# Optimization experiments

Measured on AMD Instinct MI355X. Metric: run time of the kernel, lower is better.

The kernel has to match this reference:

```python
import jax, jax.numpy as jnp
import numpy as np

LN_EPS = 1e-5

def _conv2d(x, w, b, pad):
    # x: [B,C,H,W], w: [O,I,kh,kw] -> [B,O,H,W]
    y = jax.lax.conv_general_dilated(
        x, w, window_strides=(1, 1), padding=[(pad, pad), (pad, pad)],
        dimension_numbers=('NCHW', 'OIHW', 'NCHW'))
    return y + b[None, :, None, None]

def setup_inputs() -> dict:
    key = jax.random.key(0)
    ks = jax.random.split(key, 12)
    B, C, H, W = 4, 256, 64, 64
    D = 64  # inner_projection
    s_in = 1.0 / np.sqrt(C)
    s_d1 = 1.0 / np.sqrt(D)
    s_d3 = 1.0 / np.sqrt(D * 9)
    return {
        'x':     jax.random.normal(ks[0], (B, C, H, W), jnp.float32),
        'w_in':  jax.random.normal(ks[1], (D, C, 1, 1), jnp.float32) * s_in,
        'b_in':  jnp.zeros((D,), jnp.float32),
        'wq':    jax.random.normal(ks[2], (D, D, 3, 3), jnp.float32) * s_d3,
        'bq':    jnp.zeros((D,), jnp.float32),
        'wk':    jax.random.normal(ks[3], (D, D, 3, 3), jnp.float32) * s_d3,
        'bk':    jnp.zeros((D,), jnp.float32),
        'wv':    jax.random.normal(ks[4], (D, D, 3, 3), jnp.float32) * s_d3,
        'bv':    jnp.zeros((D,), jnp.float32),
        'w_out': jax.random.normal(ks[5], (C, D, 1, 1), jnp.float32) * s_d1,
        'b_out': jnp.zeros((C,), jnp.float32),
        'gamma': jax.random.normal(ks[6], (1,), jnp.float32) * 0.1,
        'ln_w':  jnp.ones((C,), jnp.float32),
        'ln_b':  jnp.zeros((C,), jnp.float32),
    }

def _attention(q, k, v):
    # full-pixel attention, NO 1/sqrt(d) scale (matches source)
    B, C, H, W = v.shape
    N = H * W
    qf = q.reshape(B, -1, N)   # [B,d,N]
    kf = k.reshape(B, -1, N)
    vf = v.reshape(B, -1, N)
    energy = jnp.einsum('bci,bcj->bij', qf, kf)      # [B,N,N] = Q^T K
    attn = jax.nn.softmax(energy, axis=-1)
    out = jnp.einsum('bcj,bij->bci', vf, attn)        # V @ attn^T
    return out.reshape(B, C, H, W)

def _layernorm2d(x, w, b):
    # normalize over channel dim per pixel (LayerNorm2d)
    mu = jnp.mean(x, axis=1, keepdims=True)
    var = jnp.var(x, axis=1, keepdims=True)
    xn = (x - mu) * jax.lax.rsqrt(var + LN_EPS)
    return xn * w[None, :, None, None] + b[None, :, None, None]

def reference(x, w_in, b_in, wq, bq, wk, bk, wv, bv, w_out, b_out, gamma, ln_w, ln_b):
    att = _conv2d(x, w_in, b_in, 0)          # inner projection [B,D,H,W]
    q = _conv2d(att, wq, bq, 1)
    k = _conv2d(att, wk, bk, 1)
    v = _conv2d(att, wv, bv, 1)
    att = _attention(q, k, v)
    att = _conv2d(att, w_out, b_out, 0)       # outer projection [B,C,H,W]
    return _layernorm2d(gamma * x + att, ln_w, ln_b)
```

## Files before the change

### kernel.cpp

```cpp
#include <hip/hip_runtime.h>
#include <hip/hip_bf16.h>

#define BB 4
#define CC 256
#define DD 64
#define HH 64
#define WW 64
#define NN 4096
#define NSPLIT 4
#define SM_SHIFT2 92.332482616893664f
#define LOG2E 1.4426950408889634f

typedef __hip_bfloat16 bf16;
typedef __attribute__((ext_vector_type(8))) short bf16x8;
typedef __attribute__((ext_vector_type(4))) float f32x4;
typedef __attribute__((ext_vector_type(4))) short s16x4;

#define MFMA16(a, b, c) __builtin_amdgcn_mfma_f32_16x16x32_bf16(a, b, c, 0, 0, 0)

#if __has_builtin(__builtin_amdgcn_mfma_f32_16x16x16bf16_1k)
static __device__ __forceinline__ f32x4 MFMA16K(s16x4 a, s16x4 b, f32x4 c) {
  return __builtin_amdgcn_mfma_f32_16x16x16bf16_1k(a, b, c, 0, 0, 0);
}
#else
static __device__ __forceinline__ f32x4 MFMA16K(s16x4 a, s16x4 b, f32x4 c) {
  f32x4 d;
  asm("v_mfma_f32_16x16x16_bf16 %0, %1, %2, %3"
      : "=&v"(d) : "v"(a), "v"(b), "v"(c));
  return d;
}
#endif

#if __has_builtin(__builtin_amdgcn_exp2f)
#define EXP2F(x) __builtin_amdgcn_exp2f(x)
#else
#define EXP2F(x) exp2f(x)
#endif

static __device__ __forceinline__ float ldin(const void* p, size_t i, bool isb) {
  return isb ? __bfloat162float(((const bf16*)p)[i]) : ((const float*)p)[i];
}
static __device__ __forceinline__ void stout(void* p, size_t i, float v, bool isb) {
  if (isb) ((bf16*)p)[i] = __float2bfloat16(v);
  else     ((float*)p)[i] = v;
}
static __device__ __forceinline__ unsigned pack2(bf16 a, bf16 b) {
  unsigned short ua = *reinterpret_cast<unsigned short*>(&a);
  unsigned short ub = *reinterpret_cast<unsigned short*>(&b);
  return (unsigned)ua | ((unsigned)ub << 16);
}
static __device__ __forceinline__ bool probe_bf16(const unsigned* lnw) {
  return lnw[0] == 0x3F803F80u;
}

__global__ __launch_bounds__(256) void k_wt(
    const void* __restrict__ wq, const void* __restrict__ wk,
    const void* __restrict__ wv, const void* __restrict__ w_in,
    const void* __restrict__ w_out,
    bf16* __restrict__ Wth, bf16* __restrict__ Wtl,
    bf16* __restrict__ Win_h, bf16* __restrict__ Win_l,
    bf16* __restrict__ Wo_h, bf16* __restrict__ Wo_l,
    const unsigned* __restrict__ lnw) {
  const bool isb = probe_bf16(lnw);
  int u = blockIdx.x * 256 + threadIdx.x;
  if (u < 110592) {
    int c3 = u / 36864, rem = u % 36864;
    int tap = rem / 4096, r2 = rem % 4096;
    int oc = r2 >> 6, ic = r2 & 63;
    const void* w = (c3 == 0) ? wq : ((c3 == 1) ? wk : wv);
    float v = ldin(w, (size_t)oc * 576 + ic * 9 + tap, isb);
    bf16 h = __float2bfloat16(v);
    Wth[u] = h;
    Wtl[u] = __float2bfloat16(v - __bfloat162float(h));
  } else if (u < 126976) {
    int v2 = u - 110592;
    float v = ldin(w_in, v2, isb);
    bf16 h = __float2bfloat16(v);
    Win_h[v2] = h;
    Win_l[v2] = __float2bfloat16(v - __bfloat162float(h));
  } else {
    int v2 = u - 126976;
    float v = ldin(w_out, v2, isb);
    bf16 h = __float2bfloat16(v);
    Wo_h[v2] = h;
    Wo_l[v2] = __float2bfloat16(v - __bfloat162float(h));
  }
}

__global__ __launch_bounds__(256) void k_conv_in(
    const void* __restrict__ x,
    const bf16* __restrict__ Win_h, const bf16* __restrict__ Win_l,
    const void* __restrict__ bias, bf16* __restrict__ att_h,
    bf16* __restrict__ att_l, const unsigned* __restrict__ lnw) {
  __shared__ __align__(16) short Xh[32 * 64];
  __shared__ __align__(16) short Xl[32 * 64];
  const bool isb = probe_bf16(lnw);
  const int b = blockIdx.y, n0 = blockIdx.x * 32;
  const int t = threadIdx.x;
  const int w = t >> 6, lane = t & 63, quad = lane >> 4, l16 = lane & 15;
  const int l7 = l16 & 7;
  const size_t xoff = (size_t)b * CC * NN;
  f32x4 acc[2];
  #pragma unroll
  for (int nt = 0; nt < 2; ++nt)
    #pragma unroll
    for (int r = 0; r < 4; ++r)
      acc[nt][r] = ldin(bias, w * 16 + quad * 4 + r, isb);
  for (int c0 = 0; c0 < CC; c0 += 64) {
    __syncthreads();
    #pragma unroll
    for (int i = 0; i < 4; ++i) {
      int u = t + i * 256;
      int dd = u >> 5, n = u & 31;
      float v0 = ldin(x, xoff + (size_t)(c0 + 2 * dd) * NN + n0 + n, isb);
      float v1 = ldin(x, xoff + (size_t)(c0 + 2 * dd + 1) * NN + n0 + n, isb);
      bf16 h0 = __float2bfloat16(v0), h1 = __float2bfloat16(v1);
      bf16 l0 = __float2bfloat16(v0 - __bfloat162float(h0));
      bf16 l1 = __float2bfloat16(v1 - __bfloat162float(h1));
      int cs = ((dd >> 2) ^ (n & 7)) * 8 + ((2 * dd) & 7);
      *(unsigned*)&Xh[n * 64 + cs] = pack2(h0, h1);
      *(unsigned*)&Xl[n * 64 + cs] = pack2(l0, l1);
    }
    __syncthreads();
    #pragma unroll
    for (int kc = 0; kc < 2; ++kc) {
      size_t woff = (size_t)(w * 16 + l16) * 256 + c0 + kc * 32 + quad * 8;
      bf16x8 wh = *(const bf16x8*)(Win_h + woff);
      bf16x8 wl = *(const bf16x8*)(Win_l + woff);
      const int xo = ((kc * 4 + quad) ^ l7) * 8;
      #pragma unroll
      for (int nt = 0; nt < 2; ++nt) {
        int rn = nt * 16 + l16;
        bf16x8 xh = *(const bf16x8*)&Xh[rn * 64 + xo];
        bf16x8 xl = *(const bf16x8*)&Xl[rn * 64 + xo];
        acc[nt] = MFMA16(wh, xh, acc[nt]);
        acc[nt] = MFMA16(wh, xl, acc[nt]);
        acc[nt] = MFMA16(wl, xh, acc[nt]);
      }
    }
  }
  #pragma unroll
  for (int nt = 0; nt < 2; ++nt) {
    size_t off = ((size_t)b * NN + n0 + nt * 16 + l16) * DD + w * 16 + quad * 4;
    bf16 h[4], l[4];
    #pragma unroll
    for (int r = 0; r < 4; ++r) {
      float v = acc[nt][r];
      h[r] = __float2bfloat16(v);
      l[r] = __float2bfloat16(v - __bfloat162float(h[r]));
    }
    *(uint2*)&att_h[off] = make_uint2(pack2(h[0], h[1]), pack2(h[2], h[3]));
    *(uint2*)&att_l[off] = make_uint2(pack2(l[0], l[1]), pack2(l[2], l[3]));
  }
}

__global__ __launch_bounds__(256) void k_conv3(
    const bf16* __restrict__ att_h, const bf16* __restrict__ att_l,
    const bf16* __restrict__ Wth, const bf16* __restrict__ Wtl,
    const void* __restrict__ bq, const void* __restrict__ bk,
    const void* __restrict__ bv,
    bf16* __restrict__ qth, bf16* __restrict__ qtl,
    bf16* __restrict__ kth, bf16* __restrict__ ktl,
    bf16* __restrict__ vt, const unsigned* __restrict__ lnw) {
  __shared__ __align__(16) short Ah[3 * 66 * 64];
  __shared__ __align__(16) short Al[3 * 66 * 64];
  float* o_s = reinterpret_cast<float*>(Ah);
  const bool isb = probe_bf16(lnw);
  const int y = blockIdx.x, b = blockIdx.y;
  const int t = threadIdx.x;
  const int w = t >> 6, lane = t & 63, quad = lane >> 4, l16 = lane & 15;
  const uint4 z4 = make_uint4(0, 0, 0, 0);
  #pragma unroll
  for (int r = 0; r < 3; ++r) {
    int yp = y + r - 1;
    bool ok = (unsigned)yp < 64u;
    const uint4* sh = (const uint4*)(att_h + ((size_t)b * NN + (size_t)yp * 64) * DD);
    const uint4* sl = (const uint4*)(att_l + ((size_t)b * NN + (size_t)yp * 64) * DD);
    #pragma unroll
    for (int ii = 0; ii < 2; ++ii) {
      int u = t + ii * 256;
      int xx = u >> 3, ch = u & 7;
      int rr = r * 66 + xx + 1;
      uint4 vh = ok ? sh[u] : z4;
      uint4 vl = ok ? sl[u] : z4;
      int cs = (ch ^ (rr & 7)) * 8;
      *(uint4*)&Ah[rr * 64 + cs] = vh;
      *(uint4*)&Al[rr * 64 + cs] = vl;
    }
    if (t < 16) {
      int rr = r * 66 + ((t & 1) ? 65 : 0);
      int cs = (t >> 1) * 8;
      *(uint4*)&Ah[rr * 64 + cs] = z4;
      *(uint4*)&Al[rr * 64 + cs] = z4;
    }
  }
  __syncthreads();
  #pragma unroll 1
  for (int c3 = 0; c3 < 3; ++c3) {
    const void* bp = (c3 == 0) ? bq : ((c3 == 1) ? bk : bv);
    const bf16* wth = Wth + (size_t)c3 * 9 * 4096;
    const bf16* wtl = Wtl + (size_t)c3 * 9 * 4096;
    f32x4 acc[4];
    #pragma unroll
    for (int nt = 0; nt < 4; ++nt)
      #pragma unroll
      for (int r = 0; r < 4; ++r)
        acc[nt][r] = ldin(bp, w * 16 + quad * 4 + r, isb);
    #pragma unroll
    for (int tap = 0; tap < 9; ++tap) {
      const int dy = tap / 3, dx = tap % 3;
      const int woff = tap * 4096 + (w * 16 + l16) * 64 + quad * 8;
      bf16x8 wh0 = *(const bf16x8*)(wth + woff);
      bf16x8 wh1 = *(const bf16x8*)(wth + woff + 32);
      bf16x8 wl0 = *(const bf16x8*)(wtl + woff);
      bf16x8 wl1 = *(const bf16x8*)(wtl + woff + 32);
      #pragma unroll
      for (int nt = 0; nt < 4; ++nt) {
        int rr = dy * 66 + nt * 16 + l16 + dx;
        int chA = (quad ^ (rr & 7)) * 8;
        int chB = ((quad + 4) ^ (rr & 7)) * 8;
        bf16x8 ah0 = *(const bf16x8*)&Ah[rr * 64 + chA];
        bf16x8 ah1 = *(const bf16x8*)&Ah[rr * 64 + chB];
        bf16x8 al0 = *(const bf16x8*)&Al[rr * 64 + chA];
        bf16x8 al1 = *(const bf16x8*)&Al[rr * 64 + chB];
        acc[nt] = MFMA16(wh0, ah0, acc[nt]);
        acc[nt] = MFMA16(wh1, ah1, acc[nt]);
        acc[nt] = MFMA16(wh0, al0, acc[nt]);
        acc[nt] = MFMA16(wh1, al1, acc[nt]);
        acc[nt] = MFMA16(wl0, ah0, acc[nt]);
        acc[nt] = MFMA16(wl1, ah1, acc[nt]);
      }
    }
    if (c3 < 2) {
      bf16* dh = (c3 == 0) ? qth : kth;
      bf16* dl = (c3 == 0) ? qtl : ktl;
      const float qsc = (c3 == 0) ? LOG2E : 1.0f;
      const size_t rowb = (size_t)b * NN + (size_t)y * 64;
      #pragma unroll
      for (int nt = 0; nt < 4; ++nt) {
        size_t off = (rowb + nt * 16 + l16) * DD + w * 16 + quad * 4;
        bf16 h[4], l[4];
        #pragma unroll
        for (int r = 0; r < 4; ++r) {
          float v = acc[nt][r] * qsc;
          h[r] = __float2bfloat16(v);
          l[r] = __float2bfloat16(v - __bfloat162float(h[r]));
        }
        *(uint2*)&dh[off] = make_uint2(pack2(h[0], h[1]), pack2(h[2], h[3]));
        *(uint2*)&dl[off] = make_uint2(pack2(l[0], l[1]), pack2(l[2], l[3]));
      }
    } else {
      __syncthreads();
      #pragma unroll
      for (int nt = 0; nt < 4; ++nt)
        #pragma unroll
        for (int r = 0; r < 4; ++r)
          o_s[(nt * 16 + l16) * 65 + w * 16 + quad * 4 + r] = acc[nt][r];
      __syncthreads();
      #pragma unroll
      for (int i = 0; i < 8; ++i) {
        int u = t + i * 256;
        int c = u >> 5, np = (u & 31) * 2;
        float v0 = o_s[np * 65 + c], v1 = o_s[(np + 1) * 65 + c];
        *(unsigned*)&vt[((size_t)b * DD + c) * NN + (size_t)y * 64 + np] =
            pack2(__float2bfloat16(v0), __float2bfloat16(v1));
      }
    }
  }
}

__global__ __launch_bounds__(256) void k_attn(
    const bf16* __restrict__ qth, const bf16* __restrict__ qtl,
    const bf16* __restrict__ kth, const bf16* __restrict__ ktl,
    const bf16* __restrict__ vt, float* __restrict__ po,
    float* __restrict__ pl) {
  __shared__ __align__(16) short Kh[2][64 * 64];
  __shared__ __align__(16) short Kl[2][64 * 64];
  __shared__ __align__(16) short Vs[2][64 * 64];
  const int b = blockIdx.y, i0 = blockIdx.x * 128, sp = blockIdx.z;
  const int jt0 = sp * (64 / NSPLIT), jt1 = jt0 + (64 / NSPLIT);
  const int t = threadIdx.x;
  const int w = t >> 6, lane = t & 63, quad = lane >> 4, l16 = lane & 15;
  const int l7 = l16 & 7;
  const int xA = (quad ^ l7) * 8;
  const int xB = ((quad + 4) ^ l7) * 8;
  const int sr = t >> 2, m4 = t & 3, sg = m4 * 16;
  const int sc0 = ((2 * m4) ^ (sr & 7)) * 8;
  const int sc1 = ((2 * m4 + 1) ^ (sr & 7)) * 8;
  bf16x8 qf_h0[2], qf_h1[2], qf_l0[2], qf_l1[2];
  #pragma unroll
  for (int is = 0; is < 2; ++is) {
    size_t qoff = ((size_t)b * NN + i0 + is * 64 + w * 16 + l16) * DD + quad * 8;
    qf_h0[is] = *(const bf16x8*)(qth + qoff);
    qf_h1[is] = *(const bf16x8*)(qth + qoff + 32);
    qf_l0[is] = *(const bf16x8*)(qtl + qoff);
    qf_l1[is] = *(const bf16x8*)(qtl + qoff + 32);
  }
  uint4 kh0, kh1, kl0, kl1, vx0, vx1;
  {
    size_t koff = ((size_t)b * NN + jt0 * 64 + sr) * DD + sg;
    kh0 = ((const uint4*)(kth + koff))[0]; kh1 = ((const uint4*)(kth + koff))[1];
    kl0 = ((const uint4*)(ktl + koff))[0]; kl1 = ((const uint4*)(ktl + koff))[1];
    size_t voff = ((size_t)b * DD + sr) * NN + jt0 * 64 + sg;
    vx0 = ((const uint4*)(vt + voff))[0];  vx1 = ((const uint4*)(vt + voff))[1];
  }
  *(uint4*)&Kh[0][sr * 64 + sc0] = kh0;  *(uint4*)&Kh[0][sr * 64 + sc1] = kh1;
  *(uint4*)&Kl[0][sr * 64 + sc0] = kl0;  *(uint4*)&Kl[0][sr * 64 + sc1] = kl1;
  *(uint4*)&Vs[0][sr * 64 + sc0] = vx0;  *(uint4*)&Vs[0][sr * 64 + sc1] = vx1;
  __syncthreads();
  float l_run[2] = {0.f, 0.f};
  f32x4 oacc[4][2] = {};
  int p = 0;
  for (int jt = jt0; jt < jt1; ++jt) {
    if (jt < jt1 - 1) {
      int j0n = (jt + 1) * 64;
      size_t koff = ((size_t)b * NN + j0n + sr) * DD + sg;
      kh0 = ((const uint4*)(kth + koff))[0]; kh1 = ((const uint4*)(kth + koff))[1];
      kl0 = ((const uint4*)(ktl + koff))[0]; kl1 = ((const uint4*)(ktl + koff))[1];
      size_t voff = ((size_t)b * DD + sr) * NN + j0n + sg;
      vx0 = ((const uint4*)(vt + voff))[0];  vx1 = ((const uint4*)(vt + voff))[1];
    }
    const short* khp = Kh[p];
    const short* klp = Kl[p];
    const short* vsp = Vs[p];
    s16x4 pf[2][4];
    float psum[2] = {0.f, 0.f};
    #pragma unroll
    for (int mt = 0; mt < 4; ++mt) {
      int r0 = (mt * 16 + l16) * 64;
      bf16x8 kf_h0 = *(const bf16x8*)&khp[r0 + xA];
      bf16x8 kf_h1 = *(const bf16x8*)&khp[r0 + xB];
      bf16x8 kf_l0 = *(const bf16x8*)&klp[r0 + xA];
      bf16x8 kf_l1 = *(const bf16x8*)&klp[r0 + xB];
      __builtin_amdgcn_s_setprio(1);
      #pragma unroll
      for (int is = 0; is < 2; ++is) {
        f32x4 c = {0.f, 0.f, 0.f, 0.f};
        c = MFMA16(kf_h0, qf_h0[is], c);
        c = MFMA16(kf_h1, qf_h1[is], c);
        c = MFMA16(kf_h0, qf_l0[is], c);
        c = MFMA16(kf_h1, qf_l1[is], c);
        c = MFMA16(kf_l0, qf_h0[is], c);
        c = MFMA16(kf_l1, qf_h1[is], c);
        s16x4 pk;
        float ps = 0.f;
        #pragma unroll
        for (int r = 0; r < 4; ++r) {
          float pexp = EXP2F(c[r] - SM_SHIFT2);
          bf16 ph = __float2bfloat16(pexp);
          ps += __bfloat162float(ph);
          pk[r] = *reinterpret_cast<short*>(&ph);
        }
        psum[is] += ps;
        pf[is][mt] = pk;
      }
      __builtin_amdgcn_s_setprio(0);
    }
    #pragma unroll
    for (int is = 0; is < 2; ++is) {
      float ps = psum[is];
      ps += __shfl_xor(ps, 16, 64);
      ps += __shfl_xor(ps, 32, 64);
      l_run[is] += ps;
    }
    __builtin_amdgcn_s_setprio(1);
    #pragma unroll
    for (int mt = 0; mt < 4; ++mt) {
      int rv = (mt * 16 + l16) * 64;
      #pragma unroll
      for (int kt = 0; kt < 4; ++kt) {
        s16x4 vf = *(const s16x4*)
            &vsp[rv + ((kt * 2 + (quad >> 1)) ^ l7) * 8 + (quad & 1) * 4];
        oacc[mt][0] = MFMA16K(vf, pf[0][kt], oacc[mt][0]);
        oacc[mt][1] = MFMA16K(vf, pf[1][kt], oacc[mt][1]);
      }
    }
    __builtin_amdgcn_s_setprio(0);
    if (jt < jt1 - 1) {
      short* khn = Kh[p ^ 1];
      short* kln = Kl[p ^ 1];
      short* vsn = Vs[p ^ 1];
      *(uint4*)&khn[sr * 64 + sc0] = kh0;  *(uint4*)&khn[sr * 64 + sc1] = kh1;
      *(uint4*)&kln[sr * 64 + sc0] = kl0;  *(uint4*)&kln[sr * 64 + sc1] = kl1;
      *(uint4*)&vsn[sr * 64 + sc0] = vx0;  *(uint4*)&vsn[sr * 64 + sc1] = vx1;
    }
    __syncthreads();
    p ^= 1;
  }
  const size_t SEGC = (size_t)BB * DD * NN;
  #pragma unroll
  for (int is = 0; is < 2; ++is) {
    const int ig = i0 + is * 64 + w * 16 + l16;
    #pragma unroll
    for (int mt = 0; mt < 4; ++mt)
      #pragma unroll
      for (int r = 0; r < 4; ++r) {
        int c = mt * 16 + quad * 4 + r;
        po[(size_t)sp * SEGC + ((size_t)b * DD + c) * NN + ig] = oacc[mt][is][r];
      }
    if (quad == 0) pl[((size_t)sp * BB + b) * NN + ig] = l_run[is];
  }
}

__global__ __launch_bounds__(256) void k_out_ln(
    const float* __restrict__ po, const float* __restrict__ pl,
    const void* __restrict__ x,
    const bf16* __restrict__ Wo_h, const bf16* __restrict__ Wo_l,
    const void* __restrict__ bias, const void* __restrict__ gamma,
    const void* __restrict__ lw, const void* __restrict__ lb,
    void* __restrict__ out, const unsigned* __restrict__ lnw) {
  __shared__ __align__(16) short Ahs[32 * 64];
  __shared__ __align__(16) short Als[32 * 64];
  __shared__ float inv_s[32];
  __shared__ float red1[32 * 4], red2[32 * 4];
  __shared__ float mu_s[32], rs_s[32];
  __shared__ float lw_s[256], lb_s[256];
  const bool isb = probe_bf16(lnw);
  const int b = blockIdx.y, n0 = blockIdx.x * 32;
  const int t = threadIdx.x;
  const int w = t >> 6, lane = t & 63, quad = lane >> 4, l16 = lane & 15;
  const int l7 = l16 & 7;
  const size_t SEGC = (size_t)BB * DD * NN;
  if (t < 32) {
    int i = n0 + t;
    float lsum = 0.f;
    #pragma unroll
    for (int s = 0; s < NSPLIT; ++s) lsum += pl[((size_t)s * BB + b) * NN + i];
    inv_s[t] = 1.f / lsum;
  }
  lw_s[t] = ldin(lw, t, isb);
  lb_s[t] = ldin(lb, t, isb);
  const float g = ldin(gamma, 0, isb);
  __syncthreads();
  #pragma unroll
  for (int i = 0; i < 4; ++i) {
    int u = t + i * 256;
    int dd = u >> 5, n = u & 31;
    size_t base = ((size_t)b * DD + 2 * dd) * NN + n0 + n;
    float v0 = 0.f, v1 = 0.f;
    #pragma unroll
    for (int s = 0; s < NSPLIT; ++s) {
      v0 += po[(size_t)s * SEGC + base];
      v1 += po[(size_t)s * SEGC + base + NN];
    }
    float inv = inv_s[n];
    v0 *= inv; v1 *= inv;
    bf16 h0 = __float2bfloat16(v0), h1 = __float2bfloat16(v1);
    bf16 l0 = __float2bfloat16(v0 - __bfloat162float(h0));
    bf16 l1 = __float2bfloat16(v1 - __bfloat162float(h1));
    int cs = ((dd >> 2) ^ (n & 7)) * 8 + ((2 * dd) & 7);
    *(unsigned*)&Ahs[n * 64 + cs] = pack2(h0, h1);
    *(unsigned*)&Als[n * 64 + cs] = pack2(l0, l1);
  }
  f32x4 acc[4][2];
  #pragma unroll
  for (int oct = 0; oct < 4; ++oct)
    #pragma unroll
    for (int r = 0; r < 4; ++r) {
      float bo = ldin(bias, w * 64 + oct * 16 + quad * 4 + r, isb);
      #pragma unroll
      for (int nt = 0; nt < 2; ++nt) acc[oct][nt][r] = bo;
    }
  __syncthreads();
  #pragma unroll
  for (int oct = 0; oct < 4; ++oct) {
    const int base = w * 64 + oct * 16;
    #pragma unroll
    for (int kc = 0; kc < 2; ++kc) {
      size_t woff = (size_t)(base + l16) * 64 + kc * 32 + quad * 8;
      bf16x8 wh = *(const bf16x8*)(Wo_h + woff);
      bf16x8 wl = *(const bf16x8*)(Wo_l + woff);
      const int xo = ((kc * 4 + quad) ^ l7) * 8;
      #pragma unroll
      for (int nt = 0; nt < 2; ++nt) {
        int rn = nt * 16 + l16;
        bf16x8 ah = *(const bf16x8*)&Ahs[rn * 64 + xo];
        bf16x8 al = *(const bf16x8*)&Als[rn * 64 + xo];
        acc[oct][nt] = MFMA16(wh, ah, acc[oct][nt]);
        acc[oct][nt] = MFMA16(wh, al, acc[oct][nt]);
        acc[oct][nt] = MFMA16(wl, ah, acc[oct][nt]);
      }
    }
  }
  #pragma unroll
  for (int nt = 0; nt < 2; ++nt) {
    int nn = nt * 16 + l16;
    float s1 = 0.f, s2 = 0.f;
    #pragma unroll
    for (int oct = 0; oct < 4; ++oct)
      #pragma unroll
      for (int r = 0; r < 4; ++r) {
        int oc = w * 64 + oct * 16 + quad * 4 + r;
        float xv = ldin(x, ((size_t)b * CC + oc) * NN + n0 + nn, isb);
        float y = acc[oct][nt][r] + g * xv;
        acc[oct][nt][r] = y;
        s1 += y; s2 += y * y;
      }
    s1 += __shfl_xor(s1, 16, 64); s1 += __shfl_xor(s1, 32, 64);
    s2 += __shfl_xor(s2, 16, 64); s2 += __shfl_xor(s2, 32, 64);
    if (quad == 0) { red1[nn * 4 + w] = s1; red2[nn * 4 + w] = s2; }
  }
  __syncthreads();
  if (t < 32) {
    float sm = red1[t * 4] + red1[t * 4 + 1] + red1[t * 4 + 2] + red1[t * 4 + 3];
    float sq = red2[t * 4] + red2[t * 4 + 1] + red2[t * 4 + 2] + red2[t * 4 + 3];
    float mu = sm * (1.f / 256.f);
    float var = sq * (1.f / 256.f) - mu * mu;
    mu_s[t] = mu;
    rs_s[t] = rsqrtf(var + 1e-5f);
  }
  __syncthreads();
  #pragma unroll
  for (int nt = 0; nt < 2; ++nt) {
    int nn = nt * 16 + l16;
    float mu = mu_s[nn], rs = rs_s[nn];
    #pragma unroll
    for (int oct = 0; oct < 4; ++oct)
      #pragma unroll
      for (int r = 0; r < 4; ++r) {
        int oc = w * 64 + oct * 16 + quad * 4 + r;
        float o = (acc[oct][nt][r] - mu) * rs * lw_s[oc] + lb_s[oc];
        stout(out, ((size_t)b * CC + oc) * NN + n0 + nn, o, isb);
      }
  }
}

extern "C" void kernel_launch(void* const* d_in, const int* in_sizes, int n_in,
                              void* d_out, int out_size, void* d_ws, size_t ws_size,
                              hipStream_t stream) {
  const void* x     = d_in[0];
  const void* w_in  = d_in[1];
  const void* b_in  = d_in[2];
  const void* wq    = d_in[3];
  const void* bq    = d_in[4];
  const void* wk    = d_in[5];
  const void* bk    = d_in[6];
  const void* wv    = d_in[7];
  const void* bv    = d_in[8];
  const void* w_out = d_in[9];
  const void* b_out = d_in[10];
  const void* gamma = d_in[11];
  const void* ln_w  = d_in[12];
  const void* ln_b  = d_in[13];

  const size_t SEG = (size_t)BB * DD * NN;
  char*  p     = (char*)d_ws;
  bf16*  att_h = (bf16*)p;  p += SEG * 2;
  bf16*  att_l = (bf16*)p;  p += SEG * 2;
  bf16*  qth   = (bf16*)p;  p += SEG * 2;
  bf16*  qtl   = (bf16*)p;  p += SEG * 2;
  bf16*  kth   = (bf16*)p;  p += SEG * 2;
  bf16*  ktl   = (bf16*)p;  p += SEG * 2;
  bf16*  vt    = (bf16*)p;  p += SEG * 2;
  float* po    = (float*)p; p += (size_t)NSPLIT * SEG * 4;
  float* pl    = (float*)p; p += (size_t)NSPLIT * BB * NN * 4;
  bf16*  Wth   = (bf16*)p;  p += 110592 * 2;
  bf16*  Wtl   = (bf16*)p;  p += 110592 * 2;
  bf16*  Win_h = (bf16*)p;  p += 16384 * 2;
  bf16*  Win_l = (bf16*)p;  p += 16384 * 2;
  bf16*  Wo_h  = (bf16*)p;  p += 16384 * 2;
  bf16*  Wo_l  = (bf16*)p;  p += 16384 * 2;
  const unsigned* lnw = (const unsigned*)ln_w;

  k_wt<<<560, 256, 0, stream>>>(wq, wk, wv, w_in, w_out, Wth, Wtl,
                                Win_h, Win_l, Wo_h, Wo_l, lnw);
  k_conv_in<<<dim3(NN / 32, BB), 256, 0, stream>>>(x, Win_h, Win_l, b_in,
                                                   att_h, att_l, lnw);
  k_conv3<<<dim3(64, BB), 256, 0, stream>>>(att_h, att_l, Wth, Wtl,
                                            bq, bk, bv,
                                            qth, qtl, kth, ktl, vt, lnw);
  k_attn<<<dim3(NN / 128, BB, NSPLIT), 256, 0, stream>>>(qth, qtl, kth, ktl, vt,
                                                         po, pl);
  k_out_ln<<<dim3(NN / 32, BB), 256, 0, stream>>>(po, pl, x, Wo_h, Wo_l,
                                                  b_out, gamma, ln_w, ln_b,
                                                  d_out, lnw);
}
```

Measured before the change: 184.0 us.

## Split conv3 across q/k/v blocks, double attention splits, compute row sums via MFMA

The 3x3 conv kernel now launches one block per q/k/v output via grid z, which triples parallelism at the cost of reloading the input halo three times. Attention uses NSPLIT=8 for more blocks, but that doubles the partial-output traffic and the work in the reduction stage. The softmax row sums are now accumulated with an MFMA against a ones vector instead of scalar adds and shuffles. V is single-buffered in LDS with extra barriers, which frees LDS at the cost of more synchronisation.

```diff
diff --git a/kernel.cpp b/kernel.cpp
--- a/kernel.cpp
+++ b/kernel.cpp
@@ -7,7 +7,7 @@
 #define HH 64
 #define WW 64
 #define NN 4096
-#define NSPLIT 4
+#define NSPLIT 8
 #define SM_SHIFT2 92.332482616893664f
 #define LOG2E 1.4426950408889634f
 
@@ -166,7 +166,7 @@
   __shared__ __align__(16) short Al[3 * 66 * 64];
   float* o_s = reinterpret_cast<float*>(Ah);
   const bool isb = probe_bf16(lnw);
-  const int y = blockIdx.x, b = blockIdx.y;
+  const int y = blockIdx.x, b = blockIdx.y, c3 = blockIdx.z;
   const int t = threadIdx.x;
   const int w = t >> 6, lane = t & 63, quad = lane >> 4, l16 = lane & 15;
   const uint4 z4 = make_uint4(0, 0, 0, 0);
@@ -195,76 +195,73 @@
     }
   }
   __syncthreads();
-  #pragma unroll 1
-  for (int c3 = 0; c3 < 3; ++c3) {
-    const void* bp = (c3 == 0) ? bq : ((c3 == 1) ? bk : bv);
-    const bf16* wth = Wth + (size_t)c3 * 9 * 4096;
-    const bf16* wtl = Wtl + (size_t)c3 * 9 * 4096;
-    f32x4 acc[4];
+  const void* bp = (c3 == 0) ? bq : ((c3 == 1) ? bk : bv);
+  const bf16* wth = Wth + (size_t)c3 * 9 * 4096;
+  const bf16* wtl = Wtl + (size_t)c3 * 9 * 4096;
+  f32x4 acc[4];
+  #pragma unroll
+  for (int nt = 0; nt < 4; ++nt)
+    #pragma unroll
+    for (int r = 0; r < 4; ++r)
+      acc[nt][r] = ldin(bp, w * 16 + quad * 4 + r, isb);
+  #pragma unroll
+  for (int tap = 0; tap < 9; ++tap) {
+    const int dy = tap / 3, dx = tap % 3;
+    const int woff = tap * 4096 + (w * 16 + l16) * 64 + quad * 8;
+    bf16x8 wh0 = *(const bf16x8*)(wth + woff);
+    bf16x8 wh1 = *(const bf16x8*)(wth + woff + 32);
+    bf16x8 wl0 = *(const bf16x8*)(wtl + woff);
+    bf16x8 wl1 = *(const bf16x8*)(wtl + woff + 32);
+    #pragma unroll
+    for (int nt = 0; nt < 4; ++nt) {
+      int rr = dy * 66 + nt * 16 + l16 + dx;
+      int chA = (quad ^ (rr & 7)) * 8;
+      int chB = ((quad + 4) ^ (rr & 7)) * 8;
+      bf16x8 ah0 = *(const bf16x8*)&Ah[rr * 64 + chA];
+      bf16x8 ah1 = *(const bf16x8*)&Ah[rr * 64 + chB];
+      bf16x8 al0 = *(const bf16x8*)&Al[rr * 64 + chA];
+      bf16x8 al1 = *(const bf16x8*)&Al[rr * 64 + chB];
+      acc[nt] = MFMA16(wh0, ah0, acc[nt]);
+      acc[nt] = MFMA16(wh1, ah1, acc[nt]);
+      acc[nt] = MFMA16(wh0, al0, acc[nt]);
+      acc[nt] = MFMA16(wh1, al1, acc[nt]);
+      acc[nt] = MFMA16(wl0, ah0, acc[nt]);
+      acc[nt] = MFMA16(wl1, ah1, acc[nt]);
+    }
+  }
+  if (c3 < 2) {
+    bf16* dh = (c3 == 0) ? qth : kth;
+    bf16* dl = (c3 == 0) ? qtl : ktl;
+    const float qsc = (c3 == 0) ? LOG2E : 1.0f;
+    const size_t rowb = (size_t)b * NN + (size_t)y * 64;
+    #pragma unroll
+    for (int nt = 0; nt < 4; ++nt) {
+      size_t off = (rowb + nt * 16 + l16) * DD + w * 16 + quad * 4;
+      bf16 h[4], l[4];
+      #pragma unroll
+      for (int r = 0; r < 4; ++r) {
+        float v = acc[nt][r] * qsc;
+        h[r] = __float2bfloat16(v);
+        l[r] = __float2bfloat16(v - __bfloat162float(h[r]));
+      }
+      *(uint2*)&dh[off] = make_uint2(pack2(h[0], h[1]), pack2(h[2], h[3]));
+      *(uint2*)&dl[off] = make_uint2(pack2(l[0], l[1]), pack2(l[2], l[3]));
+    }
+  } else {
+    __syncthreads();
     #pragma unroll
     for (int nt = 0; nt < 4; ++nt)
       #pragma unroll
       for (int r = 0; r < 4; ++r)
-        acc[nt][r] = ldin(bp, w * 16 + quad * 4 + r, isb);
-    #pragma unroll
-    for (int tap = 0; tap < 9; ++tap) {
-      const int dy = tap / 3, dx = tap % 3;
-      const int woff = tap * 4096 + (w * 16 + l16) * 64 + quad * 8;
-      bf16x8 wh0 = *(const bf16x8*)(wth + woff);
-      bf16x8 wh1 = *(const bf16x8*)(wth + woff + 32);
-      bf16x8 wl0 = *(const bf16x8*)(wtl + woff);
-      bf16x8 wl1 = *(const bf16x8*)(wtl + woff + 32);
-      #pragma unroll
-      for (int nt = 0; nt < 4; ++nt) {
-        int rr = dy * 66 + nt * 16 + l16 + dx;
-        int chA = (quad ^ (rr & 7)) * 8;
-        int chB = ((quad + 4) ^ (rr & 7)) * 8;
-        bf16x8 ah0 = *(const bf16x8*)&Ah[rr * 64 + chA];
-        bf16x8 ah1 = *(const bf16x8*)&Ah[rr * 64 + chB];
-        bf16x8 al0 = *(const bf16x8*)&Al[rr * 64 + chA];
-        bf16x8 al1 = *(const bf16x8*)&Al[rr * 64 + chB];
-        acc[nt] = MFMA16(wh0, ah0, acc[nt]);
-        acc[nt] = MFMA16(wh1, ah1, acc[nt]);
-        acc[nt] = MFMA16(wh0, al0, acc[nt]);
-        acc[nt] = MFMA16(wh1, al1, acc[nt]);
-        acc[nt] = MFMA16(wl0, ah0, acc[nt]);
-        acc[nt] = MFMA16(wl1, ah1, acc[nt]);
-      }
-    }
-    if (c3 < 2) {
-      bf16* dh = (c3 == 0) ? qth : kth;
-      bf16* dl = (c3 == 0) ? qtl : ktl;
-      const float qsc = (c3 == 0) ? LOG2E : 1.0f;
-      const size_t rowb = (size_t)b * NN + (size_t)y * 64;
-      #pragma unroll
-      for (int nt = 0; nt < 4; ++nt) {
-        size_t off = (rowb + nt * 16 + l16) * DD + w * 16 + quad * 4;
-        bf16 h[4], l[4];
-        #pragma unroll
-        for (int r = 0; r < 4; ++r) {
-          float v = acc[nt][r] * qsc;
-          h[r] = __float2bfloat16(v);
-          l[r] = __float2bfloat16(v - __bfloat162float(h[r]));
-        }
-        *(uint2*)&dh[off] = make_uint2(pack2(h[0], h[1]), pack2(h[2], h[3]));
-        *(uint2*)&dl[off] = make_uint2(pack2(l[0], l[1]), pack2(l[2], l[3]));
-      }
-    } else {
-      __syncthreads();
-      #pragma unroll
-      for (int nt = 0; nt < 4; ++nt)
-        #pragma unroll
-        for (int r = 0; r < 4; ++r)
-          o_s[(nt * 16 + l16) * 65 + w * 16 + quad * 4 + r] = acc[nt][r];
-      __syncthreads();
-      #pragma unroll
-      for (int i = 0; i < 8; ++i) {
-        int u = t + i * 256;
-        int c = u >> 5, np = (u & 31) * 2;
-        float v0 = o_s[np * 65 + c], v1 = o_s[(np + 1) * 65 + c];
-        *(unsigned*)&vt[((size_t)b * DD + c) * NN + (size_t)y * 64 + np] =
-            pack2(__float2bfloat16(v0), __float2bfloat16(v1));
-      }
+        o_s[(nt * 16 + l16) * 65 + w * 16 + quad * 4 + r] = acc[nt][r];
+    __syncthreads();
+    #pragma unroll
+    for (int i = 0; i < 8; ++i) {
+      int u = t + i * 256;
+      int c = u >> 5, np = (u & 31) * 2;
+      float v0 = o_s[np * 65 + c], v1 = o_s[(np + 1) * 65 + c];
+      *(unsigned*)&vt[((size_t)b * DD + c) * NN + (size_t)y * 64 + np] =
+          pack2(__float2bfloat16(v0), __float2bfloat16(v1));
     }
   }
 }
@@ -276,7 +273,7 @@
     float* __restrict__ pl) {
   __shared__ __align__(16) short Kh[2][64 * 64];
   __shared__ __align__(16) short Kl[2][64 * 64];
-  __shared__ __align__(16) short Vs[2][64 * 64];
+  __shared__ __align__(16) short Vs[64 * 64];
   const int b = blockIdx.y, i0 = blockIdx.x * 128, sp = blockIdx.z;
   const int jt0 = sp * (64 / NSPLIT), jt1 = jt0 + (64 / NSPLIT);
   const int t = threadIdx.x;
@@ -306,13 +303,16 @@
   }
   *(uint4*)&Kh[0][sr * 64 + sc0] = kh0;  *(uint4*)&Kh[0][sr * 64 + sc1] = kh1;
   *(uint4*)&Kl[0][sr * 64 + sc0] = kl0;  *(uint4*)&Kl[0][sr * 64 + sc1] = kl1;
-  *(uint4*)&Vs[0][sr * 64 + sc0] = vx0;  *(uint4*)&Vs[0][sr * 64 + sc1] = vx1;
+  *(uint4*)&Vs[sr * 64 + sc0] = vx0;     *(uint4*)&Vs[sr * 64 + sc1] = vx1;
   __syncthreads();
-  float l_run[2] = {0.f, 0.f};
+  s16x4 onesf;
+  onesf[0] = onesf[1] = onesf[2] = onesf[3] = (short)0x3F80;
+  f32x4 lacc[2] = {};
   f32x4 oacc[4][2] = {};
   int p = 0;
   for (int jt = jt0; jt < jt1; ++jt) {
-    if (jt < jt1 - 1) {
+    const bool more = (jt < jt1 - 1);
+    if (more) {
       int j0n = (jt + 1) * 64;
       size_t koff = ((size_t)b * NN + j0n + sr) * DD + sg;
       kh0 = ((const uint4*)(kth + koff))[0]; kh1 = ((const uint4*)(kth + koff))[1];
@@ -322,9 +322,7 @@
     }
     const short* khp = Kh[p];
     const short* klp = Kl[p];
-    const short* vsp = Vs[p];
     s16x4 pf[2][4];
-    float psum[2] = {0.f, 0.f};
     #pragma unroll
     for (int mt = 0; mt < 4; ++mt) {
       int r0 = (mt * 16 + l16) * 64;
@@ -343,25 +341,21 @@
         c = MFMA16(kf_l0, qf_h0[is], c);
         c = MFMA16(kf_l1, qf_h1[is], c);
         s16x4 pk;
-        float ps = 0.f;
         #pragma unroll
         for (int r = 0; r < 4; ++r) {
           float pexp = EXP2F(c[r] - SM_SHIFT2);
           bf16 ph = __float2bfloat16(pexp);
-          ps += __bfloat162float(ph);
           pk[r] = *reinterpret_cast<short*>(&ph);
         }
-        psum[is] += ps;
         pf[is][mt] = pk;
       }
       __builtin_amdgcn_s_setprio(0);
     }
-    #pragma unroll
-    for (int is = 0; is < 2; ++is) {
-      float ps = psum[is];
-      ps += __shfl_xor(ps, 16, 64);
-      ps += __shfl_xor(ps, 32, 64);
-      l_run[is] += ps;
+    if (more) {
+      short* khn = Kh[p ^ 1];
+      short* kln = Kl[p ^ 1];
+      *(uint4*)&khn[sr * 64 + sc0] = kh0;  *(uint4*)&khn[sr * 64 + sc1] = kh1;
+      *(uint4*)&kln[sr * 64 + sc0] = kl0;  *(uint4*)&kln[sr * 64 + sc1] = kl1;
     }
     __builtin_amdgcn_s_setprio(1);
     #pragma unroll
@@ -370,21 +364,22 @@
       #pragma unroll
       for (int kt = 0; kt < 4; ++kt) {
         s16x4 vf = *(const s16x4*)
-            &vsp[rv + ((kt * 2 + (quad >> 1)) ^ l7) * 8 + (quad & 1) * 4];
+            &Vs[rv + ((kt * 2 + (quad >> 1)) ^ l7) * 8 + (quad & 1) * 4];
         oacc[mt][0] = MFMA16K(vf, pf[0][kt], oacc[mt][0]);
         oacc[mt][1] = MFMA16K(vf, pf[1][kt], oacc[mt][1]);
       }
     }
+    #pragma unroll
+    for (int kt = 0; kt < 4; ++kt) {
+      lacc[0] = MFMA16K(onesf, pf[0][kt], lacc[0]);
+      lacc[1] = MFMA16K(onesf, pf[1][kt], lacc[1]);
+    }
     __builtin_amdgcn_s_setprio(0);
-    if (jt < jt1 - 1) {
-      short* khn = Kh[p ^ 1];
-      short* kln = Kl[p ^ 1];
-      short* vsn = Vs[p ^ 1];
-      *(uint4*)&khn[sr * 64 + sc0] = kh0;  *(uint4*)&khn[sr * 64 + sc1] = kh1;
-      *(uint4*)&kln[sr * 64 + sc0] = kl0;  *(uint4*)&kln[sr * 64 + sc1] = kl1;
-      *(uint4*)&vsn[sr * 64 + sc0] = vx0;  *(uint4*)&vsn[sr * 64 + sc1] = vx1;
-    }
-    __syncthreads();
+    if (more) {
+      __syncthreads();
+      *(uint4*)&Vs[sr * 64 + sc0] = vx0; *(uint4*)&Vs[sr * 64 + sc1] = vx1;
+      __syncthreads();
+    }
     p ^= 1;
   }
   const size_t SEGC = (size_t)BB * DD * NN;
@@ -398,7 +393,7 @@
         int c = mt * 16 + quad * 4 + r;
         po[(size_t)sp * SEGC + ((size_t)b * DD + c) * NN + ig] = oacc[mt][is][r];
       }
-    if (quad == 0) pl[((size_t)sp * BB + b) * NN + ig] = l_run[is];
+    if (quad == 0) pl[((size_t)sp * BB + b) * NN + ig] = lacc[is][0];
   }
 }
 
@@ -566,9 +561,9 @@
                                 Win_h, Win_l, Wo_h, Wo_l, lnw);
   k_conv_in<<<dim3(NN / 32, BB), 256, 0, stream>>>(x, Win_h, Win_l, b_in,
                                                    att_h, att_l, lnw);
-  k_conv3<<<dim3(64, BB), 256, 0, stream>>>(att_h, att_l, Wth, Wtl,
-                                            bq, bk, bv,
-                                            qth, qtl, kth, ktl, vt, lnw);
+  k_conv3<<<dim3(64, BB, 3), 256, 0, stream>>>(att_h, att_l, Wth, Wtl,
+                                               bq, bk, bv,
+                                               qth, qtl, kth, ktl, vt, lnw);
   k_attn<<<dim3(NN / 128, BB, NSPLIT), 256, 0, stream>>>(qth, qtl, kth, ktl, vt,
                                                          po, pl);
   k_out_ln<<<dim3(NN / 32, BB), 256, 0, stream>>>(po, pl, x, Wo_h, Wo_l,
```

After: 179.0 us. -2.7%, faster.
